# Performance work log

Measured on AMD Instinct MI355X. Metric: run time of the kernel, lower is better.

Reference implementation:

```python
import jax, jax.numpy as jnp
import numpy as np

B, T, D, H = 2, 2048, 1024, 16
DK = D // H


def setup_inputs() -> dict:
    key = jax.random.key(0)
    ks = jax.random.split(key, 13)
    s = 1.0 / np.sqrt(D)
    return {
        "q": jax.random.normal(ks[0], (B, T, D), jnp.float32),
        "k": jax.random.normal(ks[1], (B, T, D), jnp.float32),
        "v": jax.random.normal(ks[2], (B, T, D), jnp.float32),
        "mask": jax.random.randint(ks[3], (B, T, T), 0, 2, jnp.int32),
        "Wq": jax.random.normal(ks[4], (D, D), jnp.float32) * s,
        "bq": jax.random.normal(ks[5], (D,), jnp.float32) * s,
        "Wk": jax.random.normal(ks[6], (D, D), jnp.float32) * s,
        "bk": jax.random.normal(ks[7], (D,), jnp.float32) * s,
        "Wv": jax.random.normal(ks[8], (D, D), jnp.float32) * s,
        "bv": jax.random.normal(ks[9], (D,), jnp.float32) * s,
        "Wo": jax.random.normal(ks[10], (D, D), jnp.float32) * s,
        "bo": jax.random.normal(ks[11], (D,), jnp.float32) * s,
    }


def reference(q, k, v, mask, Wq, bq, Wk, bk, Wv, bv, Wo, bo):
    # Linear projections (torch Linear: x @ W.T + b), split into heads.
    Q = (q @ Wq.T + bq).reshape(B, T, H, DK).transpose(0, 2, 1, 3)  # [B,H,Tq,dk]
    K = (k @ Wk.T + bk).reshape(B, T, H, DK).transpose(0, 2, 1, 3)
    V = (v @ Wv.T + bv).reshape(B, T, H, DK).transpose(0, 2, 1, 3)
    scores = jnp.einsum("bhqd,bhkd->bhqk", Q, K) / jnp.sqrt(jnp.float32(DK))
    # 3-dim mask path: mask==0 -> -1e9, broadcast over heads.
    scores = jnp.where(mask[:, None, :, :] == 0, jnp.float32(-1e9), scores)
    attn = jax.nn.softmax(scores, axis=-1)
    out = jnp.einsum("bhqk,bhkd->bhqd", attn, V)  # [B,H,Tq,dk]
    out = out.transpose(0, 2, 1, 3).reshape(B, T, D)
    return out @ Wo.T + bo
```

## Files before the change

kernel.cpp:

```cpp
#include <hip/hip_runtime.h>
#include <cstdint>
#include <cstddef>

#define TSEQ 2048
#define DMOD 1024
#define NHEAD 16
#define NBATCH 2
#define MT (NBATCH * TSEQ)
#define LOG2E 1.44269504088896340736f

typedef __attribute__((ext_vector_type(8))) __bf16 bf16x8;
typedef __attribute__((ext_vector_type(4))) float f32x4;
typedef __attribute__((ext_vector_type(8))) unsigned short u16x8;
typedef __attribute__((ext_vector_type(4))) unsigned short u16x4;
typedef __attribute__((ext_vector_type(4))) uint32_t u32x4;

__device__ __forceinline__ unsigned short f2bf(float f) {
  uint32_t u = __builtin_bit_cast(uint32_t, f);
  u += 0x7fffu + ((u >> 16) & 1u);
  return (unsigned short)(u >> 16);
}

__device__ __forceinline__ uint32_t cvt_pk_bf16(float a, float b) {
  uint32_t r;
  asm("v_cvt_pk_bf16_f32 %0, %1, %2" : "=v"(r) : "v"(a), "v"(b));
  return r;
}

__device__ __forceinline__ void gload_lds16(const void* g, const void* l) {
  auto gp = (const __attribute__((address_space(1))) uint32_t*)((uintptr_t)g);
  auto lp = (__attribute__((address_space(3))) uint32_t*)((uintptr_t)l);
  __builtin_amdgcn_global_load_lds(gp, lp, 16, 0, 0);
}

__global__ __launch_bounds__(256) void cvt_all(const float* __restrict__ q,
                                               const float* __restrict__ k,
                                               const float* __restrict__ v,
                                               const float* __restrict__ w0,
                                               const float* __restrict__ w1,
                                               const float* __restrict__ w2,
                                               const float* __restrict__ w3,
                                               unsigned short* __restrict__ din,
                                               unsigned short* __restrict__ dw) {
  const int y = blockIdx.y;
  const float* s;
  unsigned short* d;
  size_t n;
  if (y < 3) {
    s = y == 0 ? q : (y == 1 ? k : v);
    d = din + (size_t)y * MT * DMOD;
    n = (size_t)MT * DMOD;
  } else {
    s = y == 3 ? w0 : (y == 4 ? w1 : (y == 5 ? w2 : w3));
    d = dw + (size_t)(y - 3) * DMOD * DMOD;
    n = (size_t)DMOD * DMOD;
  }
  const size_t i = ((size_t)blockIdx.x * 256 + threadIdx.x) * 4;
  if (i >= n) return;
  const float4 t = *(const float4*)(s + i);
  u16x4 o;
  o[0] = f2bf(t.x); o[1] = f2bf(t.y); o[2] = f2bf(t.z); o[3] = f2bf(t.w);
  *(u16x4*)(d + i) = o;
}

__global__ __launch_bounds__(256) void mask_exp(const int* __restrict__ m,
                                                uint32_t* __restrict__ mx) {
  const size_t W = (size_t)blockIdx.x * 256 + threadIdx.x;
  const int hi = (int)((W >> 3) & 3), ct = (int)(W & 7);
  const size_t bqkt = W >> 5;
  const int kt = (int)(bqkt & 15);
  const size_t bq = bqkt >> 4;
  const int4 mm = *(const int4*)(m + bq * TSEQ + kt * 128 + ct * 16 + hi * 4);
  const uint32_t o = (mm.x ? 0xFFu : 0u) | (mm.y ? 0xFF00u : 0u) |
                     (mm.z ? 0xFF0000u : 0u) | (mm.w ? 0xFF000000u : 0u);
  mx[W] = o;
}

__device__ __forceinline__ void store_c(unsigned short* C, size_t idx, float v) { C[idx] = f2bf(v); }
__device__ __forceinline__ void store_c(float* C, size_t idx, float v) { C[idx] = v; }

template <typename OT, int MF>
__global__ __launch_bounds__(256) void gemm_bt(const unsigned short* __restrict__ A0,
                                               const unsigned short* __restrict__ A1,
                                               const unsigned short* __restrict__ A2,
                                               const unsigned short* __restrict__ W0,
                                               const unsigned short* __restrict__ W1,
                                               const unsigned short* __restrict__ W2,
                                               const float* __restrict__ b0,
                                               const float* __restrict__ b1,
                                               const float* __restrict__ b2,
                                               OT* __restrict__ C0, OT* __restrict__ C1, OT* __restrict__ C2,
                                               float s0, float s1, float s2) {
  constexpr int BM = MF * 32;
  constexpr int NX = 4096 / BM;
  const int nb = gridDim.x, per = nb >> 3, bid = blockIdx.x;
  const int swz = (bid & 7) * per + (bid >> 3);
  const int z = swz / (NX * 8);
  const int rem = swz % (NX * 8);
  const int m0 = (rem >> 3) * BM, n0 = (rem & 7) * 128;

  const unsigned short* A  = z == 0 ? A0 : (z == 1 ? A1 : A2);
  const unsigned short* Bw = z == 0 ? W0 : (z == 1 ? W1 : W2);
  const float* bias = z == 0 ? b0 : (z == 1 ? b1 : b2);
  OT* C = z == 0 ? C0 : (z == 1 ? C1 : C2);
  const float scale = z == 0 ? s0 : (z == 1 ? s1 : s2);

  __shared__ alignas(16) unsigned short As[2][BM * 32];
  __shared__ alignas(16) unsigned short Bs[2][128 * 32];
  const int tid = threadIdx.x;
  const int wid = tid >> 6;
  const int lane = tid & 63;
  const int lo = lane & 15, hi = lane >> 4;
  const int wr = wid >> 1, wc = wid & 1;
  f32x4 acc[MF][4] = {};

  const int r0 = tid >> 2, c8 = (tid & 3) * 8;
  auto stage = [&](int buf, int k0) {
#pragma unroll
    for (int i = 0; i < 2; ++i) {
      const int chunk = i * 256 + tid;
      if (i < MF / 2)
        gload_lds16(A + (size_t)(m0 + i * 64 + r0) * DMOD + k0 + c8,
                    (const char*)As + buf * (BM * 64) + chunk * 16);
      gload_lds16(Bw + (size_t)(n0 + i * 64 + r0) * DMOD + k0 + c8,
                  (const char*)Bs + buf * 8192 + chunk * 16);
    }
  };

  stage(0, 0);
  __syncthreads();

  for (int k0 = 0; k0 < DMOD; k0 += 32) {
    const int cur = (k0 >> 5) & 1;
    if (k0 + 32 < DMOD) stage(cur ^ 1, k0 + 32);

    bf16x8 af[MF], bfr[4];
#pragma unroll
    for (int m = 0; m < MF; ++m)
      af[m] = *(const bf16x8*)((const char*)As + cur * (BM * 64) +
                               (wr * (MF * 16) + m * 16 + lo) * 64 + hi * 16);
#pragma unroll
    for (int n = 0; n < 4; ++n)
      bfr[n] = *(const bf16x8*)((const char*)Bs + cur * 8192 +
                                (wc * 64 + n * 16 + lo) * 64 + hi * 16);
#pragma unroll
    for (int m = 0; m < MF; ++m)
#pragma unroll
      for (int n = 0; n < 4; ++n)
        acc[m][n] = __builtin_amdgcn_mfma_f32_16x16x32_bf16(af[m], bfr[n], acc[m][n], 0, 0, 0);

    __syncthreads();
  }

#pragma unroll
  for (int n = 0; n < 4; ++n) {
    const int col = n0 + wc * 64 + n * 16 + lo;
    const float bv = bias[col];
#pragma unroll
    for (int m = 0; m < MF; ++m) {
      const int row = m0 + wr * (MF * 16) + m * 16 + hi * 4;
#pragma unroll
      for (int r = 0; r < 4; ++r)
        store_c(C, (size_t)(row + r) * DMOD + col, (acc[m][n][r] + bv) * scale);
    }
  }
}

__global__ __launch_bounds__(256) void transpose_v(const unsigned short* __restrict__ Vp,
                                                   unsigned short* __restrict__ Vt) {
  __shared__ alignas(16) unsigned short tile[64][72];
  const int tid = threadIdx.x;
  const int bt0 = blockIdx.x * 64;
  const int h = blockIdx.y;
  const int b = bt0 >> 11;
  const int t0 = bt0 & (TSEQ - 1);
#pragma unroll
  for (int i = 0; i < 2; ++i) {
    const int chunk = i * 256 + tid;
    const int row = chunk >> 3, c = chunk & 7;
    *(uint4*)((char*)&tile[row][0] + c * 16) =
        *(const uint4*)(Vp + (size_t)(bt0 + row) * DMOD + h * 64 + c * 8);
  }
  __syncthreads();
#pragma unroll
  for (int i = 0; i < 2; ++i) {
    const int chunk = i * 256 + tid;
    const int dk = chunk >> 3, c = chunk & 7;
    u16x8 o;
#pragma unroll
    for (int j = 0; j < 8; ++j) {
      const int x = c * 8 + j;
      const int kl = (x & 32) | ((x & 24) >> 1) | ((x & 4) << 2) | (x & 3);
      o[j] = tile[kl][dk];
    }
    *(u16x8*)(Vt + ((size_t)(b * NHEAD + h) * 64 + dk) * TSEQ + t0 + c * 8) = o;
  }
}

__global__ __launch_bounds__(512, 4) void attn_kernel(const unsigned short* __restrict__ Qp,
                                                      const unsigned short* __restrict__ Kp,
                                                      const unsigned short* __restrict__ Vt,
                                                      const uint32_t* __restrict__ mx,
                                                      unsigned short* __restrict__ AO) {
  __shared__ alignas(16) unsigned short Ks[2][128 * 64];
  __shared__ alignas(16) unsigned short Vs[2][64 * 128];
  const int tid = threadIdx.x;
  const int w = tid >> 6, lane = tid & 63;
  const int lo = lane & 15, hi = lane >> 4;
  const int f = blockIdx.x;
  const int swz = (f & 7) * 64 + (f >> 3);
  const int q0 = (swz & 15) * 128;
  const int h = (swz >> 4) & 15;
  const int b = swz >> 8;

  bf16x8 qf[2];
  {
    const unsigned short* qsrc =
        Qp + (size_t)(b * TSEQ + q0 + w * 16 + lo) * DMOD + h * 64 + hi * 8;
    qf[0] = *(const bf16x8*)qsrc;
    qf[1] = *(const bf16x8*)(qsrc + 32);
  }

  bf16x8 ones;
  {
    u32x4 od;
    od[0] = 0x3F803F80u; od[1] = 0x3F803F80u; od[2] = 0x3F803F80u; od[3] = 0x3F803F80u;
    ones = __builtin_bit_cast(bf16x8, od);
  }

  f32x4 o_acc[4] = {};
  f32x4 l_acc = {};

  const size_t kbase = (size_t)(b * TSEQ) * DMOD + h * 64;
  const size_t vbase = (size_t)(b * NHEAD + h) * 64 * TSEQ;

  const int c0 = tid, c1 = 512 + tid;
  const unsigned short* kp0 = Kp + kbase + (size_t)(c0 >> 3) * DMOD + ((c0 & 7) ^ ((c0 >> 3) & 7)) * 8;
  const unsigned short* kp1 = Kp + kbase + (size_t)(c1 >> 3) * DMOD + ((c1 & 7) ^ ((c1 >> 3) & 7)) * 8;
  const unsigned short* vp0 = Vt + vbase + (size_t)(c0 >> 4) * TSEQ + ((c0 & 15) ^ ((c0 >> 4) & 7)) * 8;
  const unsigned short* vp1 = Vt + vbase + (size_t)(c1 >> 4) * TSEQ + ((c1 & 15) ^ ((c1 >> 4) & 7)) * 8;
  const uint32_t* mp = mx + (size_t)(b * TSEQ + q0 + w * 16 + lo) * 512 + hi * 8;
  const int wb0 = c0 * 16, wb1 = c1 * 16;

  int koffA[8], koffB[8];
#pragma unroll
  for (int ct = 0; ct < 8; ++ct) {
    const int kcol = ct * 16 + lo;
    koffA[ct] = kcol * 128 + ((hi ^ (kcol & 7)) * 16);
    koffB[ct] = kcol * 128 + (((4 + hi) ^ (kcol & 7)) * 16);
  }
  int voff[4][4];
#pragma unroll
  for (int vt = 0; vt < 4; ++vt) {
    const int dk = vt * 16 + lo;
#pragma unroll
    for (int c = 0; c < 4; ++c) voff[vt][c] = dk * 256 + (((c * 4 + hi) ^ (dk & 7)) * 16);
  }

  auto stage = [&](int buf) {
    gload_lds16(kp0, (const char*)Ks[buf] + wb0);
    gload_lds16(kp1, (const char*)Ks[buf] + wb1);
    gload_lds16(vp0, (const char*)Vs[buf] + wb0);
    gload_lds16(vp1, (const char*)Vs[buf] + wb1);
    kp0 += (size_t)128 * DMOD; kp1 += (size_t)128 * DMOD;
    vp0 += 128; vp1 += 128;
  };

  const uint32_t selA = 0x01010000u, selB = 0x03030202u;
  const int NT = TSEQ / 128;

  uint4 mc0 = *(const uint4*)mp, mc1 = *(const uint4*)(mp + 4);
  mp += 32;
  stage(0);
  __syncthreads();

  for (int kt = 0; kt < NT; ++kt) {
    uint4 mn0 = mc0, mn1 = mc1;
    if (kt + 1 < NT) {
      mn0 = *(const uint4*)mp;
      mn1 = *(const uint4*)(mp + 4);
      mp += 32;
      stage((kt + 1) & 1);
    }

    const char* ksb = (const char*)Ks[kt & 1];
    const char* vsb = (const char*)Vs[kt & 1];
    f32x4 s[8];
    __builtin_amdgcn_s_setprio(1);
#pragma unroll
    for (int ct = 0; ct < 8; ++ct) {
      bf16x8 kf0 = *(const bf16x8*)(ksb + koffA[ct]);
      bf16x8 kf1 = *(const bf16x8*)(ksb + koffB[ct]);
      f32x4 zz = {0.f, 0.f, 0.f, 0.f};
      s[ct] = __builtin_amdgcn_mfma_f32_16x16x32_bf16(kf0, qf[0], zz, 0, 0, 0);
      s[ct] = __builtin_amdgcn_mfma_f32_16x16x32_bf16(kf1, qf[1], s[ct], 0, 0, 0);
    }
    __builtin_amdgcn_s_setprio(0);

#pragma unroll
    for (int ct = 0; ct < 8; ++ct) {
      s[ct][0] = __builtin_exp2f(s[ct][0]);
      s[ct][1] = __builtin_exp2f(s[ct][1]);
      s[ct][2] = __builtin_exp2f(s[ct][2]);
      s[ct][3] = __builtin_exp2f(s[ct][3]);
    }

    bf16x8 pf[4];
#pragma unroll
    for (int c = 0; c < 4; ++c) {
      const uint32_t We = c == 0 ? mc0.x : (c == 1 ? mc0.z : (c == 2 ? mc1.x : mc1.z));
      const uint32_t Wo = c == 0 ? mc0.y : (c == 1 ? mc0.w : (c == 2 ? mc1.y : mc1.w));
      u32x4 pd;
      pd[0] = cvt_pk_bf16(s[2 * c][0], s[2 * c][1]) & __builtin_amdgcn_perm(We, We, selA);
      pd[1] = cvt_pk_bf16(s[2 * c][2], s[2 * c][3]) & __builtin_amdgcn_perm(We, We, selB);
      pd[2] = cvt_pk_bf16(s[2 * c + 1][0], s[2 * c + 1][1]) & __builtin_amdgcn_perm(Wo, Wo, selA);
      pd[3] = cvt_pk_bf16(s[2 * c + 1][2], s[2 * c + 1][3]) & __builtin_amdgcn_perm(Wo, Wo, selB);
      pf[c] = __builtin_bit_cast(bf16x8, pd);
    }

    __builtin_amdgcn_s_setprio(1);
#pragma unroll
    for (int vt = 0; vt < 4; ++vt) {
#pragma unroll
      for (int c = 0; c < 4; ++c) {
        bf16x8 vf = *(const bf16x8*)(vsb + voff[vt][c]);
        o_acc[vt] = __builtin_amdgcn_mfma_f32_16x16x32_bf16(pf[c], vf, o_acc[vt], 0, 0, 0);
      }
    }
#pragma unroll
    for (int c = 0; c < 4; ++c)
      l_acc = __builtin_amdgcn_mfma_f32_16x16x32_bf16(pf[c], ones, l_acc, 0, 0, 0);
    __builtin_amdgcn_s_setprio(0);

    __syncthreads();
    mc0 = mn0; mc1 = mn1;
  }

#pragma unroll
  for (int r = 0; r < 4; ++r) {
    const float rl = 1.0f / l_acc[r];
    const size_t orow = (size_t)(b * TSEQ + q0 + w * 16 + hi * 4 + r) * DMOD + h * 64;
#pragma unroll
    for (int vt = 0; vt < 4; ++vt)
      AO[orow + vt * 16 + lo] = f2bf(o_acc[vt][r] * rl);
  }
}

extern "C" void kernel_launch(void* const* d_in, const int* in_sizes, int n_in,
                              void* d_out, int out_size, void* d_ws, size_t ws_size,
                              hipStream_t stream) {
  const float* q  = (const float*)d_in[0];
  const float* k  = (const float*)d_in[1];
  const float* v  = (const float*)d_in[2];
  const int* mask = (const int*)d_in[3];
  const float* Wq = (const float*)d_in[4];
  const float* bq = (const float*)d_in[5];
  const float* Wk = (const float*)d_in[6];
  const float* bk = (const float*)d_in[7];
  const float* Wv = (const float*)d_in[8];
  const float* bv = (const float*)d_in[9];
  const float* Wo = (const float*)d_in[10];
  const float* bo = (const float*)d_in[11];
  float* out = (float*)d_out;

  char* ws = (char*)d_ws;
  const size_t SZ_BT = (size_t)MT * DMOD * 2;
  const size_t SZ_W  = (size_t)DMOD * DMOD * 2;

  unsigned short* qb  = (unsigned short*)(ws + 0);
  unsigned short* kb  = (unsigned short*)(ws + SZ_BT);
  unsigned short* vb  = (unsigned short*)(ws + 2 * SZ_BT);
  unsigned short* Qp  = (unsigned short*)(ws + 3 * SZ_BT);
  unsigned short* Kp  = (unsigned short*)(ws + 4 * SZ_BT);
  unsigned short* Vp  = (unsigned short*)(ws + 5 * SZ_BT);
  unsigned short* Wqb = (unsigned short*)(ws + 6 * SZ_BT);
  unsigned short* Wob = (unsigned short*)(ws + 6 * SZ_BT + 3 * SZ_W);
  unsigned short* Vt  = vb;
  unsigned short* AO  = qb;
  uint32_t*       mx  = (uint32_t*)kb;

  const int nBT = MT * DMOD;
  const int nW  = DMOD * DMOD;

  cvt_all<<<dim3(nBT / 1024, 7), 256, 0, stream>>>(q, k, v, Wq, Wk, Wv, Wo, qb, Wqb);

  const float qs = 0.125f * LOG2E;
  gemm_bt<unsigned short, 4><<<dim3(768), 256, 0, stream>>>(
      qb, kb, vb, Wqb, Wqb + nW, Wqb + 2 * nW, bq, bk, bv, Qp, Kp, Vp, qs, 1.0f, 1.0f);

  mask_exp<<<(NBATCH * TSEQ * 16 * 32) / 256, 256, 0, stream>>>(mask, mx);

  transpose_v<<<dim3(MT / 64, NHEAD), 256, 0, stream>>>(Vp, Vt);

  attn_kernel<<<dim3(512), 512, 0, stream>>>(Qp, Kp, Vt, mx, AO);

  gemm_bt<float, 2><<<dim3(512), 256, 0, stream>>>(
      AO, AO, AO, Wob, Wob, Wob, bo, bo, bo, out, out, out, 1.0f, 1.0f, 1.0f);
}
```

Before: 148.1 us.

## Fuse fp32-to-bf16 activation conversion into QKV GEMM A-tile loading

The QKV projection GEMM now reads fp32 q/k/v directly into registers, converts them to bf16 with packed cvt instructions and writes them to LDS, overlapped with the MFMA loop. This removes the separate activation conversion pass and its bf16 round trip through memory. The weight conversion and mask expansion are merged into one launch. In exchange, the GEMM reads twice the A bytes through VGPRs instead of direct global-to-LDS loads, which raises register pressure.

```diff
diff --git a/kernel.cpp b/kernel.cpp
--- a/kernel.cpp
+++ b/kernel.cpp
@@ -33,56 +33,42 @@
   __builtin_amdgcn_global_load_lds(gp, lp, 16, 0, 0);
 }
 
-__global__ __launch_bounds__(256) void cvt_all(const float* __restrict__ q,
-                                               const float* __restrict__ k,
-                                               const float* __restrict__ v,
-                                               const float* __restrict__ w0,
-                                               const float* __restrict__ w1,
-                                               const float* __restrict__ w2,
-                                               const float* __restrict__ w3,
-                                               unsigned short* __restrict__ din,
-                                               unsigned short* __restrict__ dw) {
-  const int y = blockIdx.y;
-  const float* s;
-  unsigned short* d;
-  size_t n;
-  if (y < 3) {
-    s = y == 0 ? q : (y == 1 ? k : v);
-    d = din + (size_t)y * MT * DMOD;
-    n = (size_t)MT * DMOD;
+__global__ __launch_bounds__(256) void cvt_wm(const float* __restrict__ w0,
+                                              const float* __restrict__ w1,
+                                              const float* __restrict__ w2,
+                                              const float* __restrict__ w3,
+                                              const int* __restrict__ m,
+                                              unsigned short* __restrict__ dw,
+                                              uint32_t* __restrict__ mx) {
+  const int bx = blockIdx.x;
+  if (bx < 4096) {
+    const size_t idx = ((size_t)bx * 256 + threadIdx.x) * 4;
+    const int wsel = (int)(idx >> 20);
+    const float* s = wsel == 0 ? w0 : (wsel == 1 ? w1 : (wsel == 2 ? w2 : w3));
+    const float4 t = *(const float4*)(s + (idx & 0xFFFFFu));
+    u16x4 o;
+    o[0] = f2bf(t.x); o[1] = f2bf(t.y); o[2] = f2bf(t.z); o[3] = f2bf(t.w);
+    *(u16x4*)(dw + idx) = o;
   } else {
-    s = y == 3 ? w0 : (y == 4 ? w1 : (y == 5 ? w2 : w3));
-    d = dw + (size_t)(y - 3) * DMOD * DMOD;
-    n = (size_t)DMOD * DMOD;
-  }
-  const size_t i = ((size_t)blockIdx.x * 256 + threadIdx.x) * 4;
-  if (i >= n) return;
-  const float4 t = *(const float4*)(s + i);
-  u16x4 o;
-  o[0] = f2bf(t.x); o[1] = f2bf(t.y); o[2] = f2bf(t.z); o[3] = f2bf(t.w);
-  *(u16x4*)(d + i) = o;
-}
-
-__global__ __launch_bounds__(256) void mask_exp(const int* __restrict__ m,
-                                                uint32_t* __restrict__ mx) {
-  const size_t W = (size_t)blockIdx.x * 256 + threadIdx.x;
-  const int hi = (int)((W >> 3) & 3), ct = (int)(W & 7);
-  const size_t bqkt = W >> 5;
-  const int kt = (int)(bqkt & 15);
-  const size_t bq = bqkt >> 4;
-  const int4 mm = *(const int4*)(m + bq * TSEQ + kt * 128 + ct * 16 + hi * 4);
-  const uint32_t o = (mm.x ? 0xFFu : 0u) | (mm.y ? 0xFF00u : 0u) |
-                     (mm.z ? 0xFF0000u : 0u) | (mm.w ? 0xFF000000u : 0u);
-  mx[W] = o;
+    const size_t W = (size_t)(bx - 4096) * 256 + threadIdx.x;
+    const int hi = (int)((W >> 3) & 3), ct = (int)(W & 7);
+    const size_t bqkt = W >> 5;
+    const int kt = (int)(bqkt & 15);
+    const size_t bq = bqkt >> 4;
+    const int4 mm = *(const int4*)(m + bq * TSEQ + kt * 128 + ct * 16 + hi * 4);
+    const uint32_t o = (mm.x ? 0xFFu : 0u) | (mm.y ? 0xFF00u : 0u) |
+                       (mm.z ? 0xFF0000u : 0u) | (mm.w ? 0xFF000000u : 0u);
+    mx[W] = o;
+  }
 }
 
 __device__ __forceinline__ void store_c(unsigned short* C, size_t idx, float v) { C[idx] = f2bf(v); }
 __device__ __forceinline__ void store_c(float* C, size_t idx, float v) { C[idx] = v; }
 
-template <typename OT, int MF>
-__global__ __launch_bounds__(256) void gemm_bt(const unsigned short* __restrict__ A0,
-                                               const unsigned short* __restrict__ A1,
-                                               const unsigned short* __restrict__ A2,
+template <typename OT, int MF, bool AF32>
+__global__ __launch_bounds__(256) void gemm_bt(const void* __restrict__ A0v,
+                                               const void* __restrict__ A1v,
+                                               const void* __restrict__ A2v,
                                                const unsigned short* __restrict__ W0,
                                                const unsigned short* __restrict__ W1,
                                                const unsigned short* __restrict__ W2,
@@ -99,7 +85,7 @@
   const int rem = swz % (NX * 8);
   const int m0 = (rem >> 3) * BM, n0 = (rem & 7) * 128;
 
-  const unsigned short* A  = z == 0 ? A0 : (z == 1 ? A1 : A2);
+  const void* Av = z == 0 ? A0v : (z == 1 ? A1v : A2v);
   const unsigned short* Bw = z == 0 ? W0 : (z == 1 ? W1 : W2);
   const float* bias = z == 0 ? b0 : (z == 1 ? b1 : b2);
   OT* C = z == 0 ? C0 : (z == 1 ? C1 : C2);
@@ -115,24 +101,57 @@
   f32x4 acc[MF][4] = {};
 
   const int r0 = tid >> 2, c8 = (tid & 3) * 8;
+  float4 fa[2][2];
+
+  auto loadA = [&](int k0) {
+    if constexpr (AF32) {
+#pragma unroll
+      for (int i = 0; i < 2; ++i) {
+        const int chunk = i * 256 + tid;
+        const int row = chunk >> 2, cc = (chunk & 3) * 8;
+        const float* p = (const float*)Av + (size_t)(m0 + row) * DMOD + k0 + cc;
+        fa[i][0] = *(const float4*)p;
+        fa[i][1] = *(const float4*)(p + 4);
+      }
+    }
+  };
+  auto writeA = [&](int buf) {
+    if constexpr (AF32) {
+#pragma unroll
+      for (int i = 0; i < 2; ++i) {
+        const int chunk = i * 256 + tid;
+        u32x4 o;
+        o[0] = cvt_pk_bf16(fa[i][0].x, fa[i][0].y);
+        o[1] = cvt_pk_bf16(fa[i][0].z, fa[i][0].w);
+        o[2] = cvt_pk_bf16(fa[i][1].x, fa[i][1].y);
+        o[3] = cvt_pk_bf16(fa[i][1].z, fa[i][1].w);
+        *(u32x4*)((char*)As + buf * (BM * 64) + chunk * 16) = o;
+      }
+    }
+  };
   auto stage = [&](int buf, int k0) {
 #pragma unroll
     for (int i = 0; i < 2; ++i) {
       const int chunk = i * 256 + tid;
-      if (i < MF / 2)
-        gload_lds16(A + (size_t)(m0 + i * 64 + r0) * DMOD + k0 + c8,
-                    (const char*)As + buf * (BM * 64) + chunk * 16);
+      if constexpr (!AF32) {
+        if (i < MF / 2)
+          gload_lds16((const unsigned short*)Av + (size_t)(m0 + i * 64 + r0) * DMOD + k0 + c8,
+                      (const char*)As + buf * (BM * 64) + chunk * 16);
+      }
       gload_lds16(Bw + (size_t)(n0 + i * 64 + r0) * DMOD + k0 + c8,
                   (const char*)Bs + buf * 8192 + chunk * 16);
     }
   };
 
+  loadA(0);
+  writeA(0);
   stage(0, 0);
   __syncthreads();
 
   for (int k0 = 0; k0 < DMOD; k0 += 32) {
     const int cur = (k0 >> 5) & 1;
-    if (k0 + 32 < DMOD) stage(cur ^ 1, k0 + 32);
+    const bool more = k0 + 32 < DMOD;
+    if (more) { loadA(k0 + 32); stage(cur ^ 1, k0 + 32); }
 
     bf16x8 af[MF], bfr[4];
 #pragma unroll
@@ -149,6 +168,7 @@
       for (int n = 0; n < 4; ++n)
         acc[m][n] = __builtin_amdgcn_mfma_f32_16x16x32_bf16(af[m], bfr[n], acc[m][n], 0, 0, 0);
 
+    if (more) writeA(cur ^ 1);
     __syncthreads();
   }
 
@@ -365,35 +385,29 @@
 
   char* ws = (char*)d_ws;
   const size_t SZ_BT = (size_t)MT * DMOD * 2;
-  const size_t SZ_W  = (size_t)DMOD * DMOD * 2;
-
-  unsigned short* qb  = (unsigned short*)(ws + 0);
-  unsigned short* kb  = (unsigned short*)(ws + SZ_BT);
-  unsigned short* vb  = (unsigned short*)(ws + 2 * SZ_BT);
-  unsigned short* Qp  = (unsigned short*)(ws + 3 * SZ_BT);
-  unsigned short* Kp  = (unsigned short*)(ws + 4 * SZ_BT);
-  unsigned short* Vp  = (unsigned short*)(ws + 5 * SZ_BT);
-  unsigned short* Wqb = (unsigned short*)(ws + 6 * SZ_BT);
-  unsigned short* Wob = (unsigned short*)(ws + 6 * SZ_BT + 3 * SZ_W);
-  unsigned short* Vt  = vb;
-  unsigned short* AO  = qb;
-  uint32_t*       mx  = (uint32_t*)kb;
-
-  const int nBT = MT * DMOD;
-  const int nW  = DMOD * DMOD;
-
-  cvt_all<<<dim3(nBT / 1024, 7), 256, 0, stream>>>(q, k, v, Wq, Wk, Wv, Wo, qb, Wqb);
+
+  unsigned short* Qp  = (unsigned short*)(ws + 0);
+  unsigned short* Kp  = (unsigned short*)(ws + SZ_BT);
+  unsigned short* Vp  = (unsigned short*)(ws + 2 * SZ_BT);
+  unsigned short* Vt  = (unsigned short*)(ws + 3 * SZ_BT);
+  unsigned short* Wqb = (unsigned short*)(ws + 4 * SZ_BT);
+  uint32_t*       mx  = (uint32_t*)(ws + 5 * SZ_BT);
+  unsigned short* AO  = Vp;
+  unsigned short* Wob = Wqb + 3 * DMOD * DMOD;
+
+  const int nW = DMOD * DMOD;
+
+  cvt_wm<<<dim3(4096 + (NBATCH * TSEQ * 16 * 32) / 256), 256, 0, stream>>>(
+      Wq, Wk, Wv, Wo, mask, Wqb, mx);
 
   const float qs = 0.125f * LOG2E;
-  gemm_bt<unsigned short, 4><<<dim3(768), 256, 0, stream>>>(
-      qb, kb, vb, Wqb, Wqb + nW, Wqb + 2 * nW, bq, bk, bv, Qp, Kp, Vp, qs, 1.0f, 1.0f);
-
-  mask_exp<<<(NBATCH * TSEQ * 16 * 32) / 256, 256, 0, stream>>>(mask, mx);
+  gemm_bt<unsigned short, 4, true><<<dim3(768), 256, 0, stream>>>(
+      q, k, v, Wqb, Wqb + nW, Wqb + 2 * nW, bq, bk, bv, Qp, Kp, Vp, qs, 1.0f, 1.0f);
 
   transpose_v<<<dim3(MT / 64, NHEAD), 256, 0, stream>>>(Vp, Vt);
 
   attn_kernel<<<dim3(512), 512, 0, stream>>>(Qp, Kp, Vt, mx, AO);
 
-  gemm_bt<float, 2><<<dim3(512), 256, 0, stream>>>(
+  gemm_bt<float, 2, false><<<dim3(512), 256, 0, stream>>>(
       AO, AO, AO, Wob, Wob, Wob, bo, bo, bo, out, out, out, 1.0f, 1.0f, 1.0f);
 }
```

New measurement: 140.3 us (median of 2 runs). -5.3%, faster.
